# Optimization experiments

Measured on AMD Instinct MI355X. Metric: run time of the kernel, lower is better.

Reference implementation:

```python
import jax, jax.numpy as jnp
import numpy as np

N_USERS = 100000
N_ITEMS = 200000
N_NODES = N_USERS + N_ITEMS
EMB_DIM = 64
N_LAYERS = 3
NNZ = 4000000


def setup_inputs() -> dict:
    key = jax.random.key(0)
    k1, k2, k3, k4, k5 = jax.random.split(key, 5)
    # xavier_uniform bound for [n, d] embedding
    bu = float(np.sqrt(6.0 / (N_USERS + EMB_DIM)))
    bi = float(np.sqrt(6.0 / (N_ITEMS + EMB_DIM)))
    user_table = jax.random.uniform(k1, (N_USERS, EMB_DIM), jnp.float32, -bu, bu)
    item_table = jax.random.uniform(k2, (N_ITEMS, EMB_DIM), jnp.float32, -bi, bi)
    adj_rows = jax.random.randint(k3, (NNZ,), 0, N_NODES, dtype=jnp.int32)
    adj_cols = jax.random.randint(k4, (NNZ,), 0, N_NODES, dtype=jnp.int32)
    # symmetric-normalized adjacency values are small positive floats
    adj_vals = jax.random.uniform(k5, (NNZ,), jnp.float32) * 0.1
    return {"user_table": user_table, "item_table": item_table,
            "adj_rows": adj_rows, "adj_cols": adj_cols, "adj_vals": adj_vals}


def _spmm(rows, cols, vals, x):
    # out[r] = sum_{nnz with row r} vals * x[col]  (COO SpMM)
    msgs = vals[:, None] * x[cols]                      # [nnz, D]
    return jax.ops.segment_sum(msgs, rows, num_segments=N_NODES)


def reference(user_table, item_table, adj_rows, adj_cols, adj_vals):
    # forward(adj_norm, perturb=False) in eval mode (dropout inactive)
    emb = jnp.concatenate([user_table, item_table], axis=0)  # [N, D]
    acc = emb  # running sum over layer outputs (incl. layer 0)
    cur = emb
    for _ in range(N_LAYERS):
        cur = _spmm(adj_rows, adj_cols, adj_vals, cur)
        acc = acc + cur
    all_emb = acc / (N_LAYERS + 1)  # mean over stacked layer embeddings
    user_emb = all_emb[:N_USERS]
    item_emb = all_emb[N_USERS:]
    return (user_emb, item_emb)
```

## Files before the change

kernel.cpp:

```cpp
#include <hip/hip_runtime.h>

#define N_USERS 100000
#define N_ITEMS 200000
#define N_NODES (N_USERS + N_ITEMS)
#define EMB     64
#define NNZ     4000000

#define BSHIFT 9
#define BROWS  (1 << BSHIFT)
#define NBUCK  ((N_NODES + BROWS - 1) >> BSHIFT)
#define NB2    1024

#define AGG_THR    512
#define AGG_EPT    8
#define AGG_T      (AGG_THR * AGG_EPT)
#define AGG_BLOCKS ((NNZ + AGG_T - 1) / AGG_T)

#define SEGCAP 8192
#define PITER  (SEGCAP / 512)

typedef _Float16 h4 __attribute__((ext_vector_type(4)));


__device__ __forceinline__ int wave_incl_scan(int v, int lane) {
#pragma unroll
    for (int d = 1; d < 64; d <<= 1) {
        int t = __shfl_up(v, d, 64);
        if (lane >= d) v += t;
    }
    return v;
}

__global__ __launch_bounds__(AGG_THR)
void bucket_agg_kernel(const int*   __restrict__ rows,
                       const int*   __restrict__ cols,
                       const float* __restrict__ vals,
                       int*         __restrict__ bcnt,
                       float2*      __restrict__ pay) {
    __shared__ int            cntS[NB2];
    __shared__ int            hoff[NB2];
    __shared__ int            waveTotS[8];
    __shared__ float2         payS[AGG_T];
    __shared__ unsigned short bidS[AGG_T];

    int tid  = threadIdx.x;
    int lane = tid & 63;
    int wid  = tid >> 6;
    int base = blockIdx.x * AGG_T;

    cntS[tid]       = 0;
    cntS[tid + 512] = 0;
    __syncthreads();

    unsigned pk[AGG_EPT];
#pragma unroll
    for (int j = 0; j < AGG_EPT; j++) {
        int e = base + j * AGG_THR + tid;
        pk[j] = 0xFFFFFFFFu;
        if (e < NNZ) {
            int r  = rows[e];
            int b  = r >> BSHIFT;
            int lp = atomicAdd(&cntS[b], 1);
            pk[j]  = ((unsigned)b << 21) | ((unsigned)(r & (BROWS - 1)) << 12)
                   | (unsigned)lp;
        }
    }
    __syncthreads();

    int v0 = cntS[2 * tid];
    int v1 = cntS[2 * tid + 1];
    int pv = v0 + v1;
    int incl = wave_incl_scan(pv, lane);
    if (lane == 63) waveTotS[wid] = incl;
    __syncthreads();
    int wbase = 0;
    for (int w = 0; w < wid; w++) wbase += waveTotS[w];
    int excl0 = wbase + incl - pv;
    int excl1 = excl0 + v0;

    if (2 * tid     < NBUCK && v0 > 0) hoff[2 * tid    ] = atomicAdd(&bcnt[(2 * tid    ) * 16], v0);
    if (2 * tid + 1 < NBUCK && v1 > 0) hoff[2 * tid + 1] = atomicAdd(&bcnt[(2 * tid + 1) * 16], v1);
    cntS[2 * tid]     = excl0;
    cntS[2 * tid + 1] = excl1;
    __syncthreads();

#pragma unroll
    for (int j = 0; j < AGG_EPT; j++) {
        if (pk[j] != 0xFFFFFFFFu) {
            int e   = base + j * AGG_THR + tid;
            int b   = pk[j] >> 21;
            int rl  = (pk[j] >> 12) & (BROWS - 1);
            int lp  = pk[j] & 0xFFF;
            int idx = cntS[b] + lp;
            unsigned packed = (unsigned)cols[e] | ((unsigned)rl << 19);
            payS[idx] = make_float2(__uint_as_float(packed), vals[e]);
            bidS[idx] = (unsigned short)b;
        }
    }
    __syncthreads();

    int total = NNZ - base; if (total > AGG_T) total = AGG_T;
    for (int i = tid; i < total; i += AGG_THR) {
        int b   = bidS[i];
        int pos = hoff[b] + (i - cntS[b]);
        if (pos < SEGCAP)
            pay[(size_t)b * SEGCAP + pos] = payS[i];
    }
}

__global__ void bscan_kernel(const int* __restrict__ bcnt,
                             int* __restrict__ bbase,
                             int* __restrict__ row_ptr) {
    __shared__ int s[1024];
    int tid = threadIdx.x;
    int v = 0;
    if (tid < NBUCK) {
        v = bcnt[tid * 16];
        if (v > SEGCAP) v = SEGCAP;
    }
    s[tid] = v;
    __syncthreads();
    for (int off = 1; off < 1024; off <<= 1) {
        int t = 0;
        if (tid >= off) t = s[tid - off];
        __syncthreads();
        if (tid >= off) s[tid] += t;
        __syncthreads();
    }
    if (tid < NBUCK) bbase[tid] = s[tid] - v;
    if (tid == 1023) bbase[NBUCK] = s[1023];
    if (tid == 0)    row_ptr[N_NODES] = NNZ;
}

__global__ __launch_bounds__(512)
void place_kernel(const int*    __restrict__ bcnt,
                  const int*    __restrict__ bbase,
                  const float2* __restrict__ pay,
                  int*          __restrict__ row_ptr,
                  float2*       __restrict__ edges,
                  const float*  __restrict__ user_t,
                  const float*  __restrict__ item_t,
                  _Float16*     __restrict__ eh) {
    __shared__ float2 payS[SEGCAP];
    __shared__ int    cntS[BROWS];
    __shared__ int    waveTotS[8];
    int b    = blockIdx.x;
    int tid  = threadIdx.x;
    int lane = tid & 63;
    int wid  = tid >> 6;
    int run  = bcnt[b * 16]; if (run > SEGCAP) run = SEGCAP;
    int beg  = bbase[b];
    const float2* seg = pay + (size_t)b * SEGCAP;

    cntS[tid] = 0;
    __syncthreads();

    unsigned eu[PITER]; float ev[PITER]; int elp[PITER];
#pragma unroll
    for (int j = 0; j < PITER; j++) {
        int i = j * 512 + tid;
        eu[j] = 0xFFFFFFFFu;
        if (i < run) {
            float2 p = seg[i];
            unsigned u = __float_as_uint(p.x);
            eu[j] = u;
            ev[j] = p.y;
            elp[j] = atomicAdd(&cntS[(u >> 19) & (BROWS - 1)], 1);
        }
    }
    __syncthreads();

    int v = cntS[tid];
    int incl = wave_incl_scan(v, lane);
    if (lane == 63) waveTotS[wid] = incl;
    __syncthreads();
    int wbase = 0;
    for (int w = 0; w < wid; w++) wbase += waveTotS[w];
    incl += wbase;
    cntS[tid] = incl;

    int gr = (b << BSHIFT) + tid;
    if (gr < N_NODES) row_ptr[gr] = beg + incl - v;
    __syncthreads();

#pragma unroll
    for (int j = 0; j < PITER; j++) {
        if (eu[j] != 0xFFFFFFFFu) {
            int r    = (int)((eu[j] >> 19) & (BROWS - 1));
            int base = (r == 0) ? 0 : cntS[r - 1];
            payS[base + elp[j]] = make_float2(__uint_as_float(eu[j] & 0x7FFFFu), ev[j]);
        }
    }
    __syncthreads();

    for (int i = tid; i < run; i += 512) {
        edges[beg + i] = payS[i];
    }

    int r0   = b << BSHIFT;
    int nrow = N_NODES - r0; if (nrow > BROWS) nrow = BROWS;
    if (nrow > 0) {
        int nel = nrow << 6;
        for (int i = tid; i < nel; i += 512) {
            int gr2 = r0 + (i >> 6);
            int d   = i & 63;
            float x = (gr2 < N_USERS)
                    ? user_t[(size_t)gr2 * EMB + d]
                    : item_t[(size_t)(gr2 - N_USERS) * EMB + d];
            eh[(size_t)r0 * EMB + i] = (_Float16)x;
        }
    }
}

__device__ __forceinline__ float4 row_gather_h(const int*      __restrict__ rp,
                                               const float2*   __restrict__ edges,
                                               const _Float16* __restrict__ xh,
                                               int row, int s) {
    int i   = rp[row];
    int end = rp[row + 1];
    float4 acc = make_float4(0.f, 0.f, 0.f, 0.f);
    for (; i + 3 < end; i += 4) {
        float2 e0 = edges[i];
        float2 e1 = edges[i + 1];
        float2 e2 = edges[i + 2];
        float2 e3 = edges[i + 3];
        h4 a = *(const h4*)(xh + ((size_t)__float_as_int(e0.x) << 6) + (s << 2));
        h4 b = *(const h4*)(xh + ((size_t)__float_as_int(e1.x) << 6) + (s << 2));
        h4 c = *(const h4*)(xh + ((size_t)__float_as_int(e2.x) << 6) + (s << 2));
        h4 d = *(const h4*)(xh + ((size_t)__float_as_int(e3.x) << 6) + (s << 2));
        acc.x += e0.y * (float)a.x + e1.y * (float)b.x + e2.y * (float)c.x + e3.y * (float)d.x;
        acc.y += e0.y * (float)a.y + e1.y * (float)b.y + e2.y * (float)c.y + e3.y * (float)d.y;
        acc.z += e0.y * (float)a.z + e1.y * (float)b.z + e2.y * (float)c.z + e3.y * (float)d.z;
        acc.w += e0.y * (float)a.w + e1.y * (float)b.w + e2.y * (float)c.w + e3.y * (float)d.w;
    }
    for (; i < end; ++i) {
        float2 e0 = edges[i];
        h4 a = *(const h4*)(xh + ((size_t)__float_as_int(e0.x) << 6) + (s << 2));
        acc.x += e0.y * (float)a.x;
        acc.y += e0.y * (float)a.y;
        acc.z += e0.y * (float)a.z;
        acc.w += e0.y * (float)a.w;
    }
    return acc;
}

__global__ void spmm_yh_kernel(const int*      __restrict__ rp,
                               const float2*   __restrict__ edges,
                               const _Float16* __restrict__ xh,
                               _Float16*       __restrict__ yh) {
    int t    = blockIdx.x * blockDim.x + threadIdx.x;
    int wid  = t >> 6;
    int lane = t & 63;
    int q    = lane >> 4;
    int s    = lane & 15;
    int row  = (wid << 2) + q;
    if (row >= N_NODES) return;
    float4 acc = row_gather_h(rp, edges, xh, row, s);
    h4 h = { (_Float16)acc.x, (_Float16)acc.y, (_Float16)acc.z, (_Float16)acc.w };
    *(h4*)(yh + (((size_t)row << 6) + (s << 2))) = h;
}

__global__ void spmm_fin_kernel(const int*      __restrict__ rp,
                                const float2*   __restrict__ edges,
                                const float*    __restrict__ user_t,
                                const float*    __restrict__ item_t,
                                const _Float16* __restrict__ y1h,
                                const _Float16* __restrict__ y2h,
                                float*          __restrict__ out) {
    int t    = blockIdx.x * blockDim.x + threadIdx.x;
    int wid  = t >> 6;
    int lane = t & 63;
    int q    = lane >> 4;
    int s    = lane & 15;
    int row  = (wid << 2) + q;
    if (row >= N_NODES) return;
    float4 acc = row_gather_h(rp, edges, y2h, row, s);
    size_t o = ((size_t)row << 6) + (s << 2);
    float4 ev;
    if (row < N_USERS)
        ev = *(const float4*)(user_t + o);
    else
        ev = *(const float4*)(item_t + o - ((size_t)N_USERS << 6));
    h4 v1 = *(const h4*)(y1h + o);
    h4 v2 = *(const h4*)(y2h + o);
    float4 r;
    r.x = (ev.x + (float)v1.x + (float)v2.x + acc.x) * 0.25f;
    r.y = (ev.y + (float)v1.y + (float)v2.y + acc.y) * 0.25f;
    r.z = (ev.z + (float)v1.z + (float)v2.z + acc.z) * 0.25f;
    r.w = (ev.w + (float)v1.w + (float)v2.w + acc.w) * 0.25f;
    *(float4*)(out + o) = r;
}

__global__ void init_kernel(const float* __restrict__ user_t,
                            const float* __restrict__ item_t,
                            float* __restrict__ out,
                            float* __restrict__ bufA,
                            float* __restrict__ bufB) {
    int i = blockIdx.x * blockDim.x + threadIdx.x;
    const int total4 = N_NODES * EMB / 4;
    if (i >= total4) return;
    int fi   = i * 4;
    int node = fi >> 6;
    int off  = fi & 63;
    float4 v;
    if (node < N_USERS)
        v = *(const float4*)(user_t + (size_t)node * EMB + off);
    else
        v = *(const float4*)(item_t + (size_t)(node - N_USERS) * EMB + off);
    *(float4*)(out  + fi) = v;
    *(float4*)(bufA + fi) = v;
    *(float4*)(bufB + fi) = make_float4(0.f, 0.f, 0.f, 0.f);
}

__global__ void spmm_kernel(const int*   __restrict__ rows,
                            const int*   __restrict__ cols,
                            const float* __restrict__ vals,
                            const float* __restrict__ x,
                            float*       __restrict__ y) {
    int tid  = blockIdx.x * blockDim.x + threadIdx.x;
    int e    = tid >> 6;
    int lane = tid & 63;
    if (e >= NNZ) return;
    atomicAdd(&y[(size_t)rows[e] * EMB + lane], vals[e] * x[(size_t)cols[e] * EMB + lane]);
}

__global__ void acc_zero_kernel(float* __restrict__ out,
                                const float* __restrict__ src,
                                float* __restrict__ zbuf) {
    int i = blockIdx.x * blockDim.x + threadIdx.x;
    const int total4 = N_NODES * EMB / 4;
    if (i >= total4) return;
    int fi = i * 4;
    float4 o = *(float4*)(out + fi);
    float4 s = *(const float4*)(src + fi);
    o.x += s.x; o.y += s.y; o.z += s.z; o.w += s.w;
    *(float4*)(out  + fi) = o;
    *(float4*)(zbuf + fi) = make_float4(0.f, 0.f, 0.f, 0.f);
}

__global__ void final_kernel(float* __restrict__ out,
                             const float* __restrict__ src) {
    int i = blockIdx.x * blockDim.x + threadIdx.x;
    const int total4 = N_NODES * EMB / 4;
    if (i >= total4) return;
    int fi = i * 4;
    float4 o = *(float4*)(out + fi);
    float4 s = *(const float4*)(src + fi);
    o.x = (o.x + s.x) * 0.25f;
    o.y = (o.y + s.y) * 0.25f;
    o.z = (o.z + s.z) * 0.25f;
    o.w = (o.w + s.w) * 0.25f;
    *(float4*)(out + fi) = o;
}

extern "C" void kernel_launch(void* const* d_in, const int* in_sizes, int n_in,
                              void* d_out, int out_size, void* d_ws, size_t ws_size,
                              hipStream_t stream) {
    const float* user_t = (const float*)d_in[0];
    const float* item_t = (const float*)d_in[1];
    const int*   rows   = (const int*)d_in[2];
    const int*   cols   = (const int*)d_in[3];
    const float* vals   = (const float*)d_in[4];
    float* out = (float*)d_out;

    const size_t embh_bytes  = (size_t)N_NODES * EMB * 2;
    const size_t emb_bytes   = (size_t)N_NODES * EMB * 4;
    const size_t pay_bytes   = (size_t)NBUCK * SEGCAP * 8;
    const size_t edges_bytes = (size_t)NNZ * 8;
    const size_t small_bytes = (size_t)(N_NODES + 1) * 4
                             + (size_t)NBUCK * 16 * 4
                             + (size_t)(NBUCK + 1) * 4;
    const int total4    = N_NODES * EMB / 4;
    const int ew_blocks = (total4 + 255) / 256;

    const size_t need_h = pay_bytes + 3 * embh_bytes + edges_bytes + small_bytes;
    const int spmm_blocks = (int)(((size_t)N_NODES / 4 * 64 + 255) / 256);

    if (ws_size >= need_h) {
        char* p = (char*)d_ws;
        float2*   pay     = (float2*)p;   p += pay_bytes;
        _Float16* eh      = (_Float16*)p; p += embh_bytes;
        _Float16* y1h     = (_Float16*)p; p += embh_bytes;
        _Float16* y2h     = (_Float16*)p; p += embh_bytes;
        float2*   edges   = (float2*)p;   p += edges_bytes;
        int*      row_ptr = (int*)p;      p += (size_t)(N_NODES + 1) * 4;
        int*      bcnt    = (int*)p;      p += (size_t)NBUCK * 16 * 4;
        int*      bbase   = (int*)p;

        hipMemsetAsync(bcnt, 0, (size_t)NBUCK * 16 * 4, stream);
        bucket_agg_kernel<<<AGG_BLOCKS, AGG_THR, 0, stream>>>(rows, cols, vals, bcnt, pay);
        bscan_kernel<<<1, 1024, 0, stream>>>(bcnt, bbase, row_ptr);
        place_kernel<<<NBUCK, 512, 0, stream>>>(bcnt, bbase, pay, row_ptr, edges,
                                                user_t, item_t, eh);

        spmm_yh_kernel <<<spmm_blocks, 256, 0, stream>>>(row_ptr, edges, eh,  y1h);
        spmm_yh_kernel <<<spmm_blocks, 256, 0, stream>>>(row_ptr, edges, y1h, y2h);
        spmm_fin_kernel<<<spmm_blocks, 256, 0, stream>>>(row_ptr, edges, user_t, item_t,
                                                         y1h, y2h, out);
    } else {
        char* p = (char*)d_ws;
        float* bufA = (float*)p; p += emb_bytes;
        float* bufB = (float*)p;
        const int spmmA_blocks = (int)(((size_t)NNZ * 64 + 255) / 256);
        init_kernel<<<ew_blocks, 256, 0, stream>>>(user_t, item_t, out, bufA, bufB);
        spmm_kernel<<<spmmA_blocks, 256, 0, stream>>>(rows, cols, vals, bufA, bufB);
        acc_zero_kernel<<<ew_blocks, 256, 0, stream>>>(out, bufB, bufA);
        spmm_kernel<<<spmmA_blocks, 256, 0, stream>>>(rows, cols, vals, bufB, bufA);
        acc_zero_kernel<<<ew_blocks, 256, 0, stream>>>(out, bufA, bufB);
        spmm_kernel<<<spmmA_blocks, 256, 0, stream>>>(rows, cols, vals, bufA, bufB);
        final_kernel<<<ew_blocks, 256, 0, stream>>>(out, bufB);
    }
}
```

Baseline: 556.5 us.

## Double row-bucket size to 1024 and alias payload buffer with fp16 embeddings

```diff
diff --git a/kernel.cpp b/kernel.cpp
--- a/kernel.cpp
+++ b/kernel.cpp
@@ -6,18 +6,19 @@
 #define EMB     64
 #define NNZ     4000000
 
-#define BSHIFT 9
+#define BSHIFT 10
 #define BROWS  (1 << BSHIFT)
 #define NBUCK  ((N_NODES + BROWS - 1) >> BSHIFT)
-#define NB2    1024
 
 #define AGG_THR    512
 #define AGG_EPT    8
 #define AGG_T      (AGG_THR * AGG_EPT)
 #define AGG_BLOCKS ((NNZ + AGG_T - 1) / AGG_T)
-
-#define SEGCAP 8192
-#define PITER  (SEGCAP / 512)
+#define SCAN_N     512
+
+#define SEGCAP 16384
+#define PCAP   SEGCAP
+#define PITER  (PCAP / 1024)
 
 typedef _Float16 h4 __attribute__((ext_vector_type(4)));
 
@@ -37,8 +38,8 @@
                        const float* __restrict__ vals,
                        int*         __restrict__ bcnt,
                        float2*      __restrict__ pay) {
-    __shared__ int            cntS[NB2];
-    __shared__ int            hoff[NB2];
+    __shared__ int            cntS[SCAN_N];
+    __shared__ int            hoff[SCAN_N];
     __shared__ int            waveTotS[8];
     __shared__ float2         payS[AGG_T];
     __shared__ unsigned short bidS[AGG_T];
@@ -48,8 +49,7 @@
     int wid  = tid >> 6;
     int base = blockIdx.x * AGG_T;
 
-    cntS[tid]       = 0;
-    cntS[tid + 512] = 0;
+    cntS[tid] = 0;
     __syncthreads();
 
     unsigned pk[AGG_EPT];
@@ -61,34 +61,29 @@
             int r  = rows[e];
             int b  = r >> BSHIFT;
             int lp = atomicAdd(&cntS[b], 1);
-            pk[j]  = ((unsigned)b << 21) | ((unsigned)(r & (BROWS - 1)) << 12)
+            pk[j]  = ((unsigned)b << 22) | ((unsigned)(r & (BROWS - 1)) << 12)
                    | (unsigned)lp;
         }
     }
     __syncthreads();
 
-    int v0 = cntS[2 * tid];
-    int v1 = cntS[2 * tid + 1];
-    int pv = v0 + v1;
-    int incl = wave_incl_scan(pv, lane);
+    int v    = cntS[tid];
+    int incl = wave_incl_scan(v, lane);
     if (lane == 63) waveTotS[wid] = incl;
     __syncthreads();
     int wbase = 0;
     for (int w = 0; w < wid; w++) wbase += waveTotS[w];
-    int excl0 = wbase + incl - pv;
-    int excl1 = excl0 + v0;
-
-    if (2 * tid     < NBUCK && v0 > 0) hoff[2 * tid    ] = atomicAdd(&bcnt[(2 * tid    ) * 16], v0);
-    if (2 * tid + 1 < NBUCK && v1 > 0) hoff[2 * tid + 1] = atomicAdd(&bcnt[(2 * tid + 1) * 16], v1);
-    cntS[2 * tid]     = excl0;
-    cntS[2 * tid + 1] = excl1;
+    int excl = wbase + incl - v;
+
+    if (tid < NBUCK && v > 0) hoff[tid] = atomicAdd(&bcnt[tid * 16], v);
+    cntS[tid] = excl;
     __syncthreads();
 
 #pragma unroll
     for (int j = 0; j < AGG_EPT; j++) {
         if (pk[j] != 0xFFFFFFFFu) {
             int e   = base + j * AGG_THR + tid;
-            int b   = pk[j] >> 21;
+            int b   = pk[j] >> 22;
             int rl  = (pk[j] >> 12) & (BROWS - 1);
             int lp  = pk[j] & 0xFFF;
             int idx = cntS[b] + lp;
@@ -111,7 +106,7 @@
 __global__ void bscan_kernel(const int* __restrict__ bcnt,
                              int* __restrict__ bbase,
                              int* __restrict__ row_ptr) {
-    __shared__ int s[1024];
+    __shared__ int s[512];
     int tid = threadIdx.x;
     int v = 0;
     if (tid < NBUCK) {
@@ -120,7 +115,7 @@
     }
     s[tid] = v;
     __syncthreads();
-    for (int off = 1; off < 1024; off <<= 1) {
+    for (int off = 1; off < 512; off <<= 1) {
         int t = 0;
         if (tid >= off) t = s[tid - off];
         __syncthreads();
@@ -128,11 +123,11 @@
         __syncthreads();
     }
     if (tid < NBUCK) bbase[tid] = s[tid] - v;
-    if (tid == 1023) bbase[NBUCK] = s[1023];
-    if (tid == 0)    row_ptr[N_NODES] = NNZ;
-}
-
-__global__ __launch_bounds__(512)
+    if (tid == 511) bbase[NBUCK] = s[511];
+    if (tid == 0)   row_ptr[N_NODES] = NNZ;
+}
+
+__global__ __launch_bounds__(1024)
 void place_kernel(const int*    __restrict__ bcnt,
                   const int*    __restrict__ bbase,
                   const float2* __restrict__ pay,
@@ -141,14 +136,14 @@
                   const float*  __restrict__ user_t,
                   const float*  __restrict__ item_t,
                   _Float16*     __restrict__ eh) {
-    __shared__ float2 payS[SEGCAP];
+    __shared__ float2 payS[PCAP];
     __shared__ int    cntS[BROWS];
-    __shared__ int    waveTotS[8];
+    __shared__ int    waveTotS[16];
     int b    = blockIdx.x;
     int tid  = threadIdx.x;
     int lane = tid & 63;
     int wid  = tid >> 6;
-    int run  = bcnt[b * 16]; if (run > SEGCAP) run = SEGCAP;
+    int run  = bcnt[b * 16]; if (run > PCAP) run = PCAP;
     int beg  = bbase[b];
     const float2* seg = pay + (size_t)b * SEGCAP;
 
@@ -158,7 +153,7 @@
     unsigned eu[PITER]; float ev[PITER]; int elp[PITER];
 #pragma unroll
     for (int j = 0; j < PITER; j++) {
-        int i = j * 512 + tid;
+        int i = j * 1024 + tid;
         eu[j] = 0xFFFFFFFFu;
         if (i < run) {
             float2 p = seg[i];
@@ -170,7 +165,7 @@
     }
     __syncthreads();
 
-    int v = cntS[tid];
+    int v    = cntS[tid];
     int incl = wave_incl_scan(v, lane);
     if (lane == 63) waveTotS[wid] = incl;
     __syncthreads();
@@ -193,7 +188,7 @@
     }
     __syncthreads();
 
-    for (int i = tid; i < run; i += 512) {
+    for (int i = tid; i < run; i += 1024) {
         edges[beg + i] = payS[i];
     }
 
@@ -201,7 +196,7 @@
     int nrow = N_NODES - r0; if (nrow > BROWS) nrow = BROWS;
     if (nrow > 0) {
         int nel = nrow << 6;
-        for (int i = tid; i < nel; i += 512) {
+        for (int i = tid; i < nel; i += 1024) {
             int gr2 = r0 + (i >> 6);
             int d   = i & 63;
             float x = (gr2 < N_USERS)
@@ -363,9 +358,10 @@
     const float* vals   = (const float*)d_in[4];
     float* out = (float*)d_out;
 
-    const size_t embh_bytes  = (size_t)N_NODES * EMB * 2;
-    const size_t emb_bytes   = (size_t)N_NODES * EMB * 4;
-    const size_t pay_bytes   = (size_t)NBUCK * SEGCAP * 8;
+    const size_t embh_bytes = (size_t)N_NODES * EMB * 2;
+    const size_t emb_bytes  = (size_t)N_NODES * EMB * 4;
+    const size_t pay_bytes  = (size_t)NBUCK * SEGCAP * 8;
+    const size_t r0_bytes   = (pay_bytes > embh_bytes ? pay_bytes : embh_bytes);
     const size_t edges_bytes = (size_t)NNZ * 8;
     const size_t small_bytes = (size_t)(N_NODES + 1) * 4
                              + (size_t)NBUCK * 16 * 4
@@ -373,25 +369,26 @@
     const int total4    = N_NODES * EMB / 4;
     const int ew_blocks = (total4 + 255) / 256;
 
-    const size_t need_h = pay_bytes + 3 * embh_bytes + edges_bytes + small_bytes;
+    const size_t need_h = r0_bytes + 2 * embh_bytes + edges_bytes + small_bytes;
     const int spmm_blocks = (int)(((size_t)N_NODES / 4 * 64 + 255) / 256);
 
     if (ws_size >= need_h) {
         char* p = (char*)d_ws;
-        float2*   pay     = (float2*)p;   p += pay_bytes;
-        _Float16* eh      = (_Float16*)p; p += embh_bytes;
+        char*     region0 = p;            p += r0_bytes;
         _Float16* y1h     = (_Float16*)p; p += embh_bytes;
         _Float16* y2h     = (_Float16*)p; p += embh_bytes;
         float2*   edges   = (float2*)p;   p += edges_bytes;
         int*      row_ptr = (int*)p;      p += (size_t)(N_NODES + 1) * 4;
         int*      bcnt    = (int*)p;      p += (size_t)NBUCK * 16 * 4;
         int*      bbase   = (int*)p;
+        float2*   pay = (float2*)region0;
+        _Float16* eh  = (_Float16*)region0;
 
         hipMemsetAsync(bcnt, 0, (size_t)NBUCK * 16 * 4, stream);
         bucket_agg_kernel<<<AGG_BLOCKS, AGG_THR, 0, stream>>>(rows, cols, vals, bcnt, pay);
-        bscan_kernel<<<1, 1024, 0, stream>>>(bcnt, bbase, row_ptr);
-        place_kernel<<<NBUCK, 512, 0, stream>>>(bcnt, bbase, pay, row_ptr, edges,
-                                                user_t, item_t, eh);
+        bscan_kernel<<<1, 512, 0, stream>>>(bcnt, bbase, row_ptr);
+        place_kernel<<<NBUCK, 1024, 0, stream>>>(bcnt, bbase, pay, row_ptr, edges,
+                                                 user_t, item_t, eh);
 
         spmm_yh_kernel <<<spmm_blocks, 256, 0, stream>>>(row_ptr, edges, eh,  y1h);
         spmm_yh_kernel <<<spmm_blocks, 256, 0, stream>>>(row_ptr, edges, y1h, y2h);
```

Measured after the change: 538.1 us. 3.3% less time.
